# Performance work log

Measured on AMD Instinct MI355X. Metric: run time of the kernel, lower is better.

The kernel has to match this reference:

```python
import jax, jax.numpy as jnp
import numpy as np

B, N, C, H, F = 8, 1024, 128, 4, 32  # batch, nodes, in_channels, heads, n_hidden
EDGE_P = 0.05


def setup_inputs() -> dict:
    key = jax.random.key(0)
    k1, k2, k3, k4 = jax.random.split(key, 4)
    x = jax.random.normal(k1, (B, N, C), dtype=jnp.float32)
    # torch Linear(in=C, out=H*F, bias=False); stored transposed so x @ W works
    W = jax.random.normal(k2, (C, H * F), dtype=jnp.float32) * (1.0 / np.sqrt(C))
    # attn Linear(2F -> 1, bias=False), single weight vector shared across heads
    a = jax.random.normal(k3, (2 * F,), dtype=jnp.float32) * (1.0 / np.sqrt(2 * F))
    # binary adjacency with self-loops so every row has at least one neighbor
    adj = (jax.random.uniform(k4, (N, N)) < EDGE_P).astype(jnp.int32)
    adj = jnp.maximum(adj, jnp.eye(N, dtype=jnp.int32))
    return {"x": x, "W": W, "a": a, "adj": adj}


def reference(x, W, a, adj):
    b, n, _ = x.shape
    f = a.shape[0] // 2
    h = W.shape[1] // f
    g = (x @ W).reshape(b, n, h, f)                      # (B,N,H,F)
    # attn(cat[g_i, g_j]) decomposes exactly: e_ij = lrelu(a1.g_i + a2.g_j)
    s_i = jnp.einsum('bihf,f->bih', g, a[:f])            # source-node term
    s_j = jnp.einsum('bjhf,f->bjh', g, a[f:])            # neighbor term
    e = jax.nn.leaky_relu(s_i[:, :, None, :] + s_j[:, None, :, :],
                          negative_slope=0.2)            # (B,N,N,H)
    e = jnp.where(adj[None, :, :, None] == 0, -jnp.inf, e)
    att = jax.nn.softmax(e, axis=2)                      # softmax over neighbors j
    out = jnp.einsum('bijh,bjhf->bihf', att, g)          # aggregate neighbors
    return out.reshape(b, n, h * f)                      # is_concat=True
```

## Files before the change

### kernel.cpp

```cpp
#include <hip/hip_runtime.h>
#include <hip/hip_bf16.h>
#include <math.h>

#define GB 8
#define GN 1024
#define GC 128
#define GH 4
#define GF 32
#define GHF 128
#define MAXNBR 192
#define XS_STRIDE 132

__global__ __launch_bounds__(256) void gat_gemm(
    const float* __restrict__ x, const float* __restrict__ W,
    const float* __restrict__ a, const int* __restrict__ adj,
    float* __restrict__ g, float* __restrict__ s1, float* __restrict__ s2,
    int* __restrict__ nbrl, int* __restrict__ cntl) {
  __shared__ float xs[16 * XS_STRIDE];
  const int t = threadIdx.x;
  const int base = blockIdx.x * 16;

  const float4* __restrict__ x4 = (const float4*)x;
  {
    float4 v0 = x4[base * 32 + t];
    float4 v1 = x4[base * 32 + t + 256];
    *(float4*)&xs[(t >> 5) * XS_STRIDE + (t & 31) * 4] = v0;
    *(float4*)&xs[((t + 256) >> 5) * XS_STRIDE + (t & 31) * 4] = v1;
  }
  __syncthreads();

  const int cg = t & 31;
  const int rg = t >> 5;
  const int c0 = cg * 4;
  const float4* __restrict__ W4 = (const float4*)W;

  float acc[2][4];
#pragma unroll
  for (int r = 0; r < 2; ++r)
#pragma unroll
    for (int i = 0; i < 4; ++i) acc[r][i] = 0.f;

#pragma unroll 4
  for (int kk = 0; kk < 32; ++kk) {
    const int k = kk * 4;
    float4 wf[4];
#pragma unroll
    for (int dk = 0; dk < 4; ++dk) wf[dk] = W4[(k + dk) * 32 + cg];
#pragma unroll
    for (int r = 0; r < 2; ++r) {
      float4 xf = *(const float4*)&xs[(rg * 2 + r) * XS_STRIDE + k];
#define FMA4(xc, wv)                         \
      acc[r][0] = fmaf(xc, wv.x, acc[r][0]); \
      acc[r][1] = fmaf(xc, wv.y, acc[r][1]); \
      acc[r][2] = fmaf(xc, wv.z, acc[r][2]); \
      acc[r][3] = fmaf(xc, wv.w, acc[r][3]);
      FMA4(xf.x, wf[0]) FMA4(xf.y, wf[1]) FMA4(xf.z, wf[2]) FMA4(xf.w, wf[3])
#undef FMA4
    }
  }

  const int h = cg >> 3;
  const int f0 = (cg & 7) * 4;
  float a1[4], a2[4];
#pragma unroll
  for (int i = 0; i < 4; ++i) { a1[i] = a[f0 + i]; a2[i] = a[GF + f0 + i]; }

#pragma unroll
  for (int r = 0; r < 2; ++r) {
    const int row = base + rg * 2 + r;
    *(float4*)&g[row * GHF + c0] =
        make_float4(acc[r][0], acc[r][1], acc[r][2], acc[r][3]);
    float v1 = acc[r][0] * a1[0] + acc[r][1] * a1[1] + acc[r][2] * a1[2] + acc[r][3] * a1[3];
    float v2 = acc[r][0] * a2[0] + acc[r][1] * a2[1] + acc[r][2] * a2[2] + acc[r][3] * a2[3];
    v1 += __shfl_xor(v1, 1); v1 += __shfl_xor(v1, 2); v1 += __shfl_xor(v1, 4);
    v2 += __shfl_xor(v2, 1); v2 += __shfl_xor(v2, 2); v2 += __shfl_xor(v2, 4);
    if ((cg & 7) == 0) { s1[row * GH + h] = v1; s2[row * GH + h] = v2; }
  }

  const int w = t >> 6;
  if (w < 2) {
    const int node = blockIdx.x * 2 + w;
    const int lane = t & 63;
    const int* __restrict__ arow = adj + node * GN;
    int* __restrict__ nrow = nbrl + node * MAXNBR;
    int pos0 = 0;
    for (int j0 = 0; j0 < GN; j0 += 64) {
      int v = arow[j0 + lane];
      unsigned long long m = __ballot(v != 0);
      if (v) {
        int pos = pos0 + __popcll(m & ((1ull << lane) - 1ull));
        if (pos < MAXNBR) nrow[pos] = j0 + lane;
      }
      pos0 += __popcll(m);
    }
    if (lane == 0) cntl[node] = min(pos0, MAXNBR);
  }
}

__global__ __launch_bounds__(256) void gat_attn(
    const float* __restrict__ g, const float* __restrict__ s1,
    const float* __restrict__ s2, const int* __restrict__ nbrl,
    const int* __restrict__ cntl, float* __restrict__ out) {
  const int bi = blockIdx.x;
  const int b = bi >> 10;
  const int i = bi & (GN - 1);
  const int t = threadIdx.x;

  __shared__ int nbr[MAXNBR];
  __shared__ float p[GH][MAXNBR];

  const int count = cntl[i];
  if (t < count) nbr[t] = nbrl[i * MAXNBR + t];
  __syncthreads();

  const int h = t >> 6;
  const int lane = t & 63;

  const float si = s1[(b * GN + i) * GH + h];
  const float* __restrict__ s2b = s2 + (size_t)b * GN * GH;
  const float* __restrict__ gb = g + (size_t)b * GN * GHF;

  float e[3];
  float m = -INFINITY;
#pragma unroll
  for (int ii = 0; ii < 3; ++ii) {
    int k = lane + ii * 64;
    if (k < count) {
      int j = nbr[k];
      float v = si + s2b[j * GH + h];
      v = v > 0.f ? v : 0.2f * v;
      e[ii] = v;
      m = fmaxf(m, v);
    }
  }
#pragma unroll
  for (int mk = 32; mk; mk >>= 1) m = fmaxf(m, __shfl_xor(m, mk));

  float s = 0.f;
#pragma unroll
  for (int ii = 0; ii < 3; ++ii) {
    int k = lane + ii * 64;
    if (k < count) {
      float pv = __expf(e[ii] - m);
      p[h][k] = pv;
      s += pv;
    }
  }
#pragma unroll
  for (int mk = 32; mk; mk >>= 1) s += __shfl_xor(s, mk);

  const int kslot = lane >> 3;
  const int f4 = lane & 7;
  float4 acc = make_float4(0.f, 0.f, 0.f, 0.f);
  for (int k = kslot; k < count; k += 8) {
    const int j = nbr[k];
    const float pv = p[h][k];
    const float4 gv = *(const float4*)&gb[(j * GH + h) * GF + f4 * 4];
    acc.x = fmaf(pv, gv.x, acc.x);
    acc.y = fmaf(pv, gv.y, acc.y);
    acc.z = fmaf(pv, gv.z, acc.z);
    acc.w = fmaf(pv, gv.w, acc.w);
  }
#pragma unroll
  for (int mk = 8; mk <= 32; mk <<= 1) {
    acc.x += __shfl_xor(acc.x, mk);
    acc.y += __shfl_xor(acc.y, mk);
    acc.z += __shfl_xor(acc.z, mk);
    acc.w += __shfl_xor(acc.w, mk);
  }
  if (kslot == 0) {
    const float inv = 1.f / s;
    *(float4*)&out[((size_t)(b * GN + i) * GH + h) * GF + f4 * 4] =
        make_float4(acc.x * inv, acc.y * inv, acc.z * inv, acc.w * inv);
  }
}

extern "C" void kernel_launch(void* const* d_in, const int* in_sizes, int n_in,
                              void* d_out, int out_size, void* d_ws, size_t ws_size,
                              hipStream_t stream) {
  const float* x = (const float*)d_in[0];
  const float* W = (const float*)d_in[1];
  const float* a = (const float*)d_in[2];
  const int* adj = (const int*)d_in[3];
  float* out = (float*)d_out;

  float* ws = (float*)d_ws;
  float* g = ws;
  float* s1 = g + (size_t)GB * GN * GH * GF;
  float* s2 = s1 + (size_t)GB * GN * GH;
  int* nbrl = (int*)(s2 + (size_t)GB * GN * GH);
  int* cntl = nbrl + (size_t)GN * MAXNBR;

  gat_gemm<<<(GB * GN) / 16, 256, 0, stream>>>(x, W, a, adj, g, s1, s2, nbrl, cntl);
  gat_attn<<<GB * GN, 256, 0, stream>>>(g, s1, s2, nbrl, cntl, out);
}
```

Baseline: 99.55 us.

## Process two batches per attention block with swizzled block order and packed p/j smem

The attention kernel now handles two batch elements per block. The neighbor list is loaded into registers once and reused for both softmax/aggregation passes, halving block count and neighbor-list reloads. Block IDs are remapped so consecutive blocks map to different batch pairs, which spreads traffic across the g slices. The softmax weight and neighbor index are packed as a float2 in shared memory so the aggregation loop does one LDS per neighbor. The GEMM inner loop unroll is raised to 8. This trades fewer, longer blocks for less redundant index loading.

```diff
diff --git a/kernel.cpp b/kernel.cpp
--- a/kernel.cpp
+++ b/kernel.cpp
@@ -40,7 +40,7 @@
 #pragma unroll
     for (int i = 0; i < 4; ++i) acc[r][i] = 0.f;
 
-#pragma unroll 4
+#pragma unroll 8
   for (int kk = 0; kk < 32; ++kk) {
     const int k = kk * 4;
     float4 wf[4];
@@ -101,13 +101,14 @@
     const float* __restrict__ g, const float* __restrict__ s1,
     const float* __restrict__ s2, const int* __restrict__ nbrl,
     const int* __restrict__ cntl, float* __restrict__ out) {
-  const int bi = blockIdx.x;
-  const int b = bi >> 10;
-  const int i = bi & (GN - 1);
+  const int bid = blockIdx.x;
+  const int wid = ((bid & 7) << 9) | (bid >> 3);
+  const int bp = wid >> 10;
+  const int i = wid & (GN - 1);
   const int t = threadIdx.x;
 
   __shared__ int nbr[MAXNBR];
-  __shared__ float p[GH][MAXNBR];
+  __shared__ float2 pj[GH][MAXNBR];
 
   const int count = cntl[i];
   if (t < count) nbr[t] = nbrl[i * MAXNBR + t];
@@ -115,63 +116,74 @@
 
   const int h = t >> 6;
   const int lane = t & 63;
-
-  const float si = s1[(b * GN + i) * GH + h];
-  const float* __restrict__ s2b = s2 + (size_t)b * GN * GH;
-  const float* __restrict__ gb = g + (size_t)b * GN * GHF;
-
-  float e[3];
-  float m = -INFINITY;
+  const int kslot = lane >> 3;
+  const int f4 = lane & 7;
+
+  int jr[3];
 #pragma unroll
   for (int ii = 0; ii < 3; ++ii) {
     int k = lane + ii * 64;
-    if (k < count) {
-      int j = nbr[k];
-      float v = si + s2b[j * GH + h];
-      v = v > 0.f ? v : 0.2f * v;
-      e[ii] = v;
-      m = fmaxf(m, v);
-    }
-  }
-#pragma unroll
-  for (int mk = 32; mk; mk >>= 1) m = fmaxf(m, __shfl_xor(m, mk));
-
-  float s = 0.f;
-#pragma unroll
-  for (int ii = 0; ii < 3; ++ii) {
-    int k = lane + ii * 64;
-    if (k < count) {
-      float pv = __expf(e[ii] - m);
-      p[h][k] = pv;
-      s += pv;
-    }
-  }
-#pragma unroll
-  for (int mk = 32; mk; mk >>= 1) s += __shfl_xor(s, mk);
-
-  const int kslot = lane >> 3;
-  const int f4 = lane & 7;
-  float4 acc = make_float4(0.f, 0.f, 0.f, 0.f);
-  for (int k = kslot; k < count; k += 8) {
-    const int j = nbr[k];
-    const float pv = p[h][k];
-    const float4 gv = *(const float4*)&gb[(j * GH + h) * GF + f4 * 4];
-    acc.x = fmaf(pv, gv.x, acc.x);
-    acc.y = fmaf(pv, gv.y, acc.y);
-    acc.z = fmaf(pv, gv.z, acc.z);
-    acc.w = fmaf(pv, gv.w, acc.w);
-  }
-#pragma unroll
-  for (int mk = 8; mk <= 32; mk <<= 1) {
-    acc.x += __shfl_xor(acc.x, mk);
-    acc.y += __shfl_xor(acc.y, mk);
-    acc.z += __shfl_xor(acc.z, mk);
-    acc.w += __shfl_xor(acc.w, mk);
-  }
-  if (kslot == 0) {
-    const float inv = 1.f / s;
-    *(float4*)&out[((size_t)(b * GN + i) * GH + h) * GF + f4 * 4] =
-        make_float4(acc.x * inv, acc.y * inv, acc.z * inv, acc.w * inv);
+    jr[ii] = (k < count) ? nbr[k] : 0;
+  }
+
+#pragma unroll
+  for (int bb = 0; bb < 2; ++bb) {
+    const int b = bp * 2 + bb;
+    const float si = s1[((size_t)b * GN + i) * GH + h];
+    const float* __restrict__ s2b = s2 + (size_t)b * GN * GH;
+    const float* __restrict__ gb = g + (size_t)b * GN * GHF;
+
+    float e[3];
+    float m = -INFINITY;
+#pragma unroll
+    for (int ii = 0; ii < 3; ++ii) {
+      int k = lane + ii * 64;
+      if (k < count) {
+        float v = si + s2b[jr[ii] * GH + h];
+        v = v > 0.f ? v : 0.2f * v;
+        e[ii] = v;
+        m = fmaxf(m, v);
+      }
+    }
+#pragma unroll
+    for (int mk = 32; mk; mk >>= 1) m = fmaxf(m, __shfl_xor(m, mk));
+
+    float s = 0.f;
+#pragma unroll
+    for (int ii = 0; ii < 3; ++ii) {
+      int k = lane + ii * 64;
+      if (k < count) {
+        float pv = __expf(e[ii] - m);
+        pj[h][k] = make_float2(pv, __int_as_float(jr[ii]));
+        s += pv;
+      }
+    }
+#pragma unroll
+    for (int mk = 32; mk; mk >>= 1) s += __shfl_xor(s, mk);
+
+    float4 acc = make_float4(0.f, 0.f, 0.f, 0.f);
+    for (int k = kslot; k < count; k += 8) {
+      const float2 v = pj[h][k];
+      const int j = __float_as_int(v.y);
+      const float pv = v.x;
+      const float4 gv = *(const float4*)&gb[(j * GH + h) * GF + f4 * 4];
+      acc.x = fmaf(pv, gv.x, acc.x);
+      acc.y = fmaf(pv, gv.y, acc.y);
+      acc.z = fmaf(pv, gv.z, acc.z);
+      acc.w = fmaf(pv, gv.w, acc.w);
+    }
+#pragma unroll
+    for (int mk = 8; mk <= 32; mk <<= 1) {
+      acc.x += __shfl_xor(acc.x, mk);
+      acc.y += __shfl_xor(acc.y, mk);
+      acc.z += __shfl_xor(acc.z, mk);
+      acc.w += __shfl_xor(acc.w, mk);
+    }
+    if (kslot == 0) {
+      const float inv = 1.f / s;
+      *(float4*)&out[(((size_t)b * GN + i) * GH + h) * GF + f4 * 4] =
+          make_float4(acc.x * inv, acc.y * inv, acc.z * inv, acc.w * inv);
+    }
   }
 }
 
@@ -192,5 +204,5 @@
   int* cntl = nbrl + (size_t)GN * MAXNBR;
 
   gat_gemm<<<(GB * GN) / 16, 256, 0, stream>>>(x, W, a, adj, g, s1, s2, nbrl, cntl);
-  gat_attn<<<GB * GN, 256, 0, stream>>>(g, s1, s2, nbrl, cntl, out);
+  gat_attn<<<(GB * GN) / 2, 256, 0, stream>>>(g, s1, s2, nbrl, cntl, out);
 }
```

After: 106.7 us. +7.1%, slower.
